# Optimization experiments

Hardware: AMD Instinct MI355X
Metric: run time of the kernel (lower is better)

Reference implementation:

```python
import jax, jax.numpy as jnp
import numpy as np

N_NODES = 50000
N_GRAPHS = 512


def _gcn_layer(x, src, dst, W, b):
    # DGL GraphConv, norm='both', allow_zero_in_degree=True
    n = x.shape[0]
    ones = jnp.ones(src.shape[0], x.dtype)
    deg_out = jnp.zeros(n, x.dtype).at[src].add(ones)
    deg_in = jnp.zeros(n, x.dtype).at[dst].add(ones)
    norm_out = jax.lax.rsqrt(jnp.maximum(deg_out, 1.0))
    norm_in = jax.lax.rsqrt(jnp.maximum(deg_in, 1.0))
    h = x * norm_out[:, None]
    agg = jax.ops.segment_sum(h[src], dst, num_segments=n)  # SpMM
    return (agg * norm_in[:, None]) @ W + b


def setup_inputs() -> dict:
    key = jax.random.key(0)
    ks = jax.random.split(key, 16)
    E = 800000
    inp = {
        'nid': jax.random.randint(ks[0], (N_NODES,), 0, 100000),
        'z': jax.random.randint(ks[1], (N_NODES,), 0, 1000),
        'src': jax.random.randint(ks[2], (E,), 0, N_NODES),
        'dst': jax.random.randint(ks[3], (E,), 0, N_NODES),
        'graph_id': jnp.sort(jax.random.randint(ks[4], (N_NODES,), 0, N_GRAPHS)),
        'init_embed': jax.random.normal(ks[5], (100000, 64), jnp.float32) * 0.1,
        'z_table': jax.random.normal(ks[6], (1000, 64), jnp.float32) * 0.1,
        'W0': jax.random.normal(ks[7], (128, 128), jnp.float32) * 0.1,
        'b0': jnp.zeros((128,), jnp.float32),
        'W1': jax.random.normal(ks[8], (128, 128), jnp.float32) * 0.1,
        'b1': jnp.zeros((128,), jnp.float32),
        'W2': jax.random.normal(ks[9], (128, 128), jnp.float32) * 0.1,
        'b2': jnp.zeros((128,), jnp.float32),
        'lin1_W': jax.random.normal(ks[10], (128, 128), jnp.float32) * 0.1,
        'lin1_b': jnp.zeros((128,), jnp.float32),
        'lin2_W': jax.random.normal(ks[11], (128, 200), jnp.float32) * 0.1,
        'lin2_b': jnp.zeros((200,), jnp.float32),
    }
    return inp


def reference(nid, z, src, dst, graph_id, init_embed, z_table, W0, b0, W1, b1, W2, b2, lin1_W, lin1_b, lin2_W, lin2_b):
    # node features: entity embedding lookup + structural label embedding, concat
    x = jnp.concatenate([init_embed[nid], z_table[z]], axis=1)  # [N, 128]
    # layers[:-1] with relu (dropout is identity in eval mode)
    x = jax.nn.relu(_gcn_layer(x, src, dst, W0, b0))
    x = jax.nn.relu(_gcn_layer(x, src, dst, W1, b1))
    x = _gcn_layer(x, src, dst, W2, b2)
    # SumPooling over subgraphs in the batch
    g = jax.ops.segment_sum(x, graph_id, num_segments=N_GRAPHS)  # [G, 128]
    h = jax.nn.relu(g @ lin1_W + lin1_b)
    return h @ lin2_W + lin2_b  # [G, num_rel]
```

## Files before the change

### kernel.cpp

```cpp
#include <hip/hip_runtime.h>
#include <hip/hip_bf16.h>


#define FEAT 128
#define NG 512
#define CH 128
#define NPMAX 12544
#define LDW 136

typedef __attribute__((ext_vector_type(8))) short bf16x8;
typedef __attribute__((ext_vector_type(4))) float f32x4;

__device__ __forceinline__ float bf2f(unsigned short u) {
    union { unsigned int i; float f; } v; v.i = ((unsigned int)u) << 16; return v.f;
}
__device__ __forceinline__ unsigned short f2bf(float f) {
    unsigned int u = __float_as_uint(f);
    return (unsigned short)((u + 0x7FFFu + ((u >> 16) & 1u)) >> 16);
}
__device__ __forceinline__ float lo16(unsigned u) { return __uint_as_float(u << 16); }
__device__ __forceinline__ float hi16(unsigned u) { return __uint_as_float(u & 0xFFFF0000u); }

__global__ __launch_bounds__(256) void k_hist(
        const int* __restrict__ src, const int* __restrict__ dst,
        unsigned* __restrict__ partial_out, unsigned* __restrict__ partial_in,
        int E, int NP, int Ec) {
    __shared__ unsigned h[NPMAX];
    int tid = threadIdx.x;
    int b = blockIdx.x;
    int c = b & (CH - 1);
    const int* __restrict__ arr = (b < CH) ? src : dst;
    unsigned* __restrict__ outp = ((b < CH) ? partial_out : partial_in) + (size_t)c * NP;
    for (int i = tid; i < NP; i += 256) h[i] = 0;
    __syncthreads();
    int e0 = c * Ec, e1 = min(E, e0 + Ec);
    for (int e = e0 + tid; e < e1; e += 256) {
        int v = arr[e];
        atomicAdd(&h[v >> 2], 1u << ((v & 3) * 8));
    }
    __syncthreads();
    for (int i = tid; i < NP; i += 256) outp[i] = h[i];
}

__global__ void k_merge(unsigned* __restrict__ partial_out, unsigned* __restrict__ partial_in,
                        int* __restrict__ cnt_in, float* __restrict__ norm_out,
                        float* __restrict__ norm_in, int N, int NP) {
    int w = blockIdx.x * blockDim.x + threadIdx.x;
    if (w >= NP) return;
    unsigned run_in = 0, run_out = 0;
    for (int c = 0; c < CH; c++) {
        size_t idx = (size_t)c * NP + w;
        unsigned v = partial_in[idx];
        partial_in[idx] = run_in;
        run_in += v;
        run_out += partial_out[idx];
    }
    #pragma unroll
    for (int j = 0; j < 4; j++) {
        int node = w * 4 + j;
        if (node < N) {
            unsigned di = (run_in  >> (j * 8)) & 255u;
            unsigned dd = (run_out >> (j * 8)) & 255u;
            cnt_in[node]   = (int)di;
            norm_in[node]  = rsqrtf(fmaxf((float)di, 1.0f));
            norm_out[node] = rsqrtf(fmaxf((float)dd, 1.0f));
        }
    }
}

__global__ void k_scan_local(const int* __restrict__ cnt, int* __restrict__ excl,
                             int* __restrict__ bsum, int N) {
    __shared__ int s[256];
    int x = threadIdx.x;
    int i = blockIdx.x * 256 + x;
    int v = (i < N) ? cnt[i] : 0;
    s[x] = v;
    __syncthreads();
    for (int off = 1; off < 256; off <<= 1) {
        int t = (x >= off) ? s[x - off] : 0;
        __syncthreads();
        s[x] += t;
        __syncthreads();
    }
    if (i < N) excl[i] = s[x] - v;
    if (x == 255) bsum[blockIdx.x] = s[255];
}

__global__ void k_scan_bsum_prep(int* __restrict__ bsum, int* __restrict__ boff, int nb,
                                 const float* __restrict__ W0, const float* __restrict__ W1,
                                 unsigned short* __restrict__ Wt0, unsigned short* __restrict__ Wt1) {
    if (blockIdx.x == 0) {
        __shared__ int s[256];
        int x = threadIdx.x;
        int v = (x < nb) ? bsum[x] : 0;
        s[x] = v;
        __syncthreads();
        for (int off = 1; off < 256; off <<= 1) {
            int t = (x >= off) ? s[x - off] : 0;
            __syncthreads();
            s[x] += t;
            __syncthreads();
        }
        if (x < nb) boff[x] = s[x] - v;
    } else {
        int t = ((int)blockIdx.x - 1) * 256 + threadIdx.x;
        if (t < 16384) {
            int n = t & 127, k = t >> 7;
            Wt0[n * 128 + k] = f2bf(W0[k * 128 + n]);
        } else {
            int t2 = t - 16384;
            int n = t2 & 127, k = t2 >> 7;
            Wt1[n * 128 + k] = f2bf(W1[k * 128 + n]);
        }
    }
}

__global__ void k_add_off(int* __restrict__ row_start, const int* __restrict__ boff, int N) {
    int i = blockIdx.x * blockDim.x + threadIdx.x;
    if (i < N) row_start[i] += boff[i >> 8];
}

__global__ __launch_bounds__(256) void k_fill_bx(
        const int* __restrict__ src, const int* __restrict__ dst,
        const int* __restrict__ row_start, const unsigned* __restrict__ partial_in,
        int* __restrict__ csr,
        const int* __restrict__ nid, const int* __restrict__ z,
        const float* __restrict__ emb, const float* __restrict__ zt,
        const float* __restrict__ nout, unsigned short* __restrict__ x,
        int N, int E, int NP, int Ec) {
    if ((int)blockIdx.x < CH) {
        __shared__ unsigned cur[NPMAX];
        int tid = threadIdx.x;
        int c = blockIdx.x;
        const unsigned* __restrict__ pre = partial_in + (size_t)c * NP;
        for (int i = tid; i < NP; i += 256) cur[i] = pre[i];
        __syncthreads();
        int e0 = c * Ec, e1 = min(E, e0 + Ec);
        for (int e = e0 + tid; e < e1; e += 256) {
            int d = dst[e], s = src[e];
            int sh = (d & 3) * 8;
            unsigned t = atomicAdd(&cur[d >> 2], 1u << sh);
            int off = (int)((t >> sh) & 255u);
            csr[row_start[d] + off] = s;
        }
    } else {
        int tid = ((int)blockIdx.x - CH) * 256 + threadIdx.x;
        int i = tid >> 5, q = tid & 31;
        if (i < N) {
            float4 v;
            if (q < 16) v = ((const float4*)emb)[(size_t)nid[i] * 16 + q];
            else        v = ((const float4*)zt)[(size_t)z[i] * 16 + (q - 16)];
            float w = nout[i];
            ushort4 u;
            u.x = f2bf(v.x * w); u.y = f2bf(v.y * w);
            u.z = f2bf(v.z * w); u.w = f2bf(v.w * w);
            ((ushort4*)x)[(size_t)i * 32 + q] = u;
        }
    }
}

#define GATHER_BODY                                                              \
    int tid = threadIdx.x;                                                       \
    int node = blockIdx.x * 16 + (tid >> 4);                                     \
    int ql = tid & 15;                                                           \
    if (node >= N) return;                                                       \
    int base = row_start[node];                                                  \
    int n = cnt_in[node];                                                        \
    float a0 = 0.f, a1 = 0.f, a2 = 0.f, a3 = 0.f;                                \
    float a4 = 0.f, a5 = 0.f, a6 = 0.f, a7 = 0.f;                                \
    const uint4* xp = (const uint4*)x;                       \
    for (int j0 = 0; j0 < n; j0 += 16) {                                         \
        int rem = n - j0;                                                        \
        int m = rem < 16 ? rem : 16;                                             \
        int e = csr[base + j0 + (ql < m ? ql : 0)];                              \
        int j = 0;                                                               \
        for (; j + 4 <= m; j += 4) {                                             \
            int s0 = __shfl(e, j + 0, 16), s1 = __shfl(e, j + 1, 16);            \
            int s2 = __shfl(e, j + 2, 16), s3 = __shfl(e, j + 3, 16);            \
            uint4 u0 = xp[(size_t)s0 * 16 + ql];                                 \
            uint4 u1 = xp[(size_t)s1 * 16 + ql];                                 \
            uint4 u2 = xp[(size_t)s2 * 16 + ql];                                 \
            uint4 u3 = xp[(size_t)s3 * 16 + ql];                                 \
            a0 += lo16(u0.x); a1 += hi16(u0.x); a2 += lo16(u0.y); a3 += hi16(u0.y); \
            a4 += lo16(u0.z); a5 += hi16(u0.z); a6 += lo16(u0.w); a7 += hi16(u0.w); \
            a0 += lo16(u1.x); a1 += hi16(u1.x); a2 += lo16(u1.y); a3 += hi16(u1.y); \
            a4 += lo16(u1.z); a5 += hi16(u1.z); a6 += lo16(u1.w); a7 += hi16(u1.w); \
            a0 += lo16(u2.x); a1 += hi16(u2.x); a2 += lo16(u2.y); a3 += hi16(u2.y); \
            a4 += lo16(u2.z); a5 += hi16(u2.z); a6 += lo16(u2.w); a7 += hi16(u2.w); \
            a0 += lo16(u3.x); a1 += hi16(u3.x); a2 += lo16(u3.y); a3 += hi16(u3.y); \
            a4 += lo16(u3.z); a5 += hi16(u3.z); a6 += lo16(u3.w); a7 += hi16(u3.w); \
        }                                                                        \
        for (; j < m; j++) {                                                     \
            int s = __shfl(e, j, 16);                                            \
            uint4 u = xp[(size_t)s * 16 + ql];                                   \
            a0 += lo16(u.x); a1 += hi16(u.x); a2 += lo16(u.y); a3 += hi16(u.y);  \
            a4 += lo16(u.z); a5 += hi16(u.z); a6 += lo16(u.w); a7 += hi16(u.w);  \
        }                                                                        \
    }                                                                            \
    float ni = nin[node];

__global__ __launch_bounds__(256) void k_gather_b(
        const unsigned short* __restrict__ x, const float* __restrict__ nin,
        const int* __restrict__ csr, const int* __restrict__ row_start,
        const int* __restrict__ cnt_in, unsigned short* __restrict__ aggB, int N) {
    GATHER_BODY
    uint4 o;
    o.x = (unsigned)f2bf(a0 * ni) | ((unsigned)f2bf(a1 * ni) << 16);
    o.y = (unsigned)f2bf(a2 * ni) | ((unsigned)f2bf(a3 * ni) << 16);
    o.z = (unsigned)f2bf(a4 * ni) | ((unsigned)f2bf(a5 * ni) << 16);
    o.w = (unsigned)f2bf(a6 * ni) | ((unsigned)f2bf(a7 * ni) << 16);
    ((uint4*)aggB)[(size_t)node * 16 + ql] = o;
}

__global__ __launch_bounds__(256) void k_gather(
        const unsigned short* __restrict__ x, const float* __restrict__ nin,
        const int* __restrict__ csr, const int* __restrict__ row_start,
        const int* __restrict__ cnt_in, float* __restrict__ agg, int N) {
    GATHER_BODY
    float4* ap = (float4*)(agg + (size_t)node * FEAT + ql * 8);
    ap[0] = make_float4(a0 * ni, a1 * ni, a2 * ni, a3 * ni);
    ap[1] = make_float4(a4 * ni, a5 * ni, a6 * ni, a7 * ni);
}

__global__ __launch_bounds__(256) void k_gemm_mfma(
        const unsigned short* __restrict__ aggB, const unsigned short* __restrict__ Wt,
        const float* __restrict__ bias, const float* __restrict__ nout,
        unsigned short* __restrict__ y, int N) {
    __shared__ unsigned short As[64 * LDW];
    __shared__ unsigned short Ws[128 * LDW];
    int tid = threadIdx.x;
    int nb = blockIdx.x * 64;

    for (int i = tid; i < 64 * 16; i += 256) {
        int row = i >> 4, seg = i & 15;
        int node = nb + row;
        ushort4 u0 = {0, 0, 0, 0}, u1 = u0;
        if (node < N) {
            const ushort4* p = (const ushort4*)(aggB + (size_t)node * 128 + seg * 8);
            u0 = p[0]; u1 = p[1];
        }
        ushort4* d = (ushort4*)(As + row * LDW + seg * 8);
        d[0] = u0; d[1] = u1;
    }
    for (int i = tid; i < 128 * 16; i += 256) {
        int row = i >> 4, seg = i & 15;
        const ushort4* p = (const ushort4*)(Wt + row * 128 + seg * 8);
        ushort4* d = (ushort4*)(Ws + row * LDW + seg * 8);
        d[0] = p[0]; d[1] = p[1];
    }
    __syncthreads();

    int lane = tid & 63;
    int m0 = (tid >> 6) * 16;
    int c = lane & 15, q = lane >> 4;

    const unsigned short* ap = As + (m0 + c) * LDW + q * 8;
    bf16x8 a0 = *(const bf16x8*)(ap);
    bf16x8 a1 = *(const bf16x8*)(ap + 32);
    bf16x8 a2 = *(const bf16x8*)(ap + 64);
    bf16x8 a3 = *(const bf16x8*)(ap + 96);

    #pragma unroll
    for (int nt = 0; nt < 8; nt++) {
        const unsigned short* wp = Ws + (nt * 16 + c) * LDW + q * 8;
        bf16x8 b0 = *(const bf16x8*)(wp);
        bf16x8 b1 = *(const bf16x8*)(wp + 32);
        bf16x8 b2 = *(const bf16x8*)(wp + 64);
        bf16x8 b3 = *(const bf16x8*)(wp + 96);
        float bb = bias[nt * 16 + c];
        f32x4 acc = {bb, bb, bb, bb};
        acc = __builtin_amdgcn_mfma_f32_16x16x32_bf16(a0, b0, acc, 0, 0, 0);
        acc = __builtin_amdgcn_mfma_f32_16x16x32_bf16(a1, b1, acc, 0, 0, 0);
        acc = __builtin_amdgcn_mfma_f32_16x16x32_bf16(a2, b2, acc, 0, 0, 0);
        acc = __builtin_amdgcn_mfma_f32_16x16x32_bf16(a3, b3, acc, 0, 0, 0);
        #pragma unroll
        for (int r = 0; r < 4; r++) {
            int row = m0 + q * 4 + r;
            float s = nout[min(nb + row, N - 1)];
            As[row * LDW + nt * 16 + c] = f2bf(fmaxf(acc[r], 0.f) * s);
        }
    }
    __syncthreads();

    for (int i = tid; i < 64 * 16; i += 256) {
        int row = i >> 4, seg = i & 15;
        int node = nb + row;
        if (node < N) {
            const ushort4* p = (const ushort4*)(As + row * LDW + seg * 8);
            ushort4* d = (ushort4*)(y + (size_t)node * 128 + seg * 8);
            d[0] = p[0]; d[1] = p[1];
        }
    }
}

__global__ __launch_bounds__(256) void k_head(
        const float* __restrict__ agg, const int* __restrict__ gid,
        const float* __restrict__ W2, const float* __restrict__ b2,
        const float* __restrict__ l1W, const float* __restrict__ l1b,
        const float* __restrict__ l2W, const float* __restrict__ l2b,
        float* __restrict__ out, int N) {
    __shared__ float g2[2][128];
    __shared__ float gs[128];
    __shared__ float ys[128];
    __shared__ float hs[128];
    int gi = blockIdx.x, tid = threadIdx.x;

    int lo = 0, hi = N;
    while (lo < hi) { int m = (lo + hi) >> 1; if (gid[m] < gi) lo = m + 1; else hi = m; }
    int s0 = lo;
    lo = 0; hi = N;
    while (lo < hi) { int m = (lo + hi) >> 1; if (gid[m] < gi + 1) lo = m + 1; else hi = m; }
    int e0 = lo;
    float cnt = (float)(e0 - s0);

    int t = tid >> 7, j = tid & 127;
    float p = 0.f;
    for (int i = s0 + t; i < e0; i += 2) p += agg[(size_t)i * FEAT + j];
    g2[t][j] = p;
    __syncthreads();
    if (tid < 128) gs[tid] = g2[0][tid] + g2[1][tid];
    __syncthreads();
    if (tid < 128) {
        float a = cnt * b2[tid];
        for (int k = 0; k < 128; k++) a += gs[k] * W2[(size_t)k * 128 + tid];
        ys[tid] = a;
    }
    __syncthreads();
    if (tid < 128) {
        float a = l1b[tid];
        for (int k = 0; k < 128; k++) a += ys[k] * l1W[(size_t)k * 128 + tid];
        hs[tid] = fmaxf(a, 0.f);
    }
    __syncthreads();
    if (tid < 200) {
        float a = l2b[tid];
        for (int k = 0; k < 128; k++) a += hs[k] * l2W[(size_t)k * 200 + tid];
        out[(size_t)gi * 200 + tid] = a;
    }
}

extern "C" void kernel_launch(void* const* d_in, const int* in_sizes, int n_in,
                              void* d_out, int out_size, void* d_ws, size_t ws_size,
                              hipStream_t stream) {
    const int*   nid = (const int*)d_in[0];
    const int*   z   = (const int*)d_in[1];
    const int*   src = (const int*)d_in[2];
    const int*   dst = (const int*)d_in[3];
    const int*   gid = (const int*)d_in[4];
    const float* emb = (const float*)d_in[5];
    const float* zt  = (const float*)d_in[6];
    const float* W0  = (const float*)d_in[7];
    const float* b0  = (const float*)d_in[8];
    const float* W1  = (const float*)d_in[9];
    const float* b1  = (const float*)d_in[10];
    const float* W2  = (const float*)d_in[11];
    const float* b2  = (const float*)d_in[12];
    const float* l1W = (const float*)d_in[13];
    const float* l1b = (const float*)d_in[14];
    const float* l2W = (const float*)d_in[15];
    const float* l2b = (const float*)d_in[16];
    float* out = (float*)d_out;

    const int N = in_sizes[0];
    const int E = in_sizes[2];
    const int NB = (N + 255) / 256;
    const int NP = (N + 3) / 4;
    const int Ec = (E + CH - 1) / CH;

    size_t NA = (size_t)((N + 63) & ~63);
    float* norm_out = (float*)d_ws;
    float* norm_in  = norm_out + NA;
    float* agg = norm_in + NA;
    unsigned short* xA   = (unsigned short*)(agg + (size_t)N * FEAT);
    unsigned short* xB   = xA + (size_t)N * FEAT;
    unsigned short* aggB = xB + (size_t)N * FEAT;
    unsigned short* Wt0  = aggB + (size_t)N * FEAT;
    unsigned short* Wt1  = Wt0 + 128 * 128;
    int* cnt_in    = (int*)(Wt1 + 128 * 128);
    int* row_start = cnt_in + NA;
    int* bsum      = row_start + NA;
    int* boff      = bsum + 256;
    unsigned* partial_out = (unsigned*)(boff + 256);
    unsigned* partial_in  = partial_out + (size_t)CH * NP;
    int* csr       = (int*)(partial_in + (size_t)CH * NP);

    k_hist<<<2 * CH, 256, 0, stream>>>(src, dst, partial_out, partial_in, E, NP, Ec);
    k_merge<<<(NP + 255) / 256, 256, 0, stream>>>(partial_out, partial_in, cnt_in,
                                                  norm_out, norm_in, N, NP);
    k_scan_local<<<NB, 256, 0, stream>>>(cnt_in, row_start, bsum, N);
    k_scan_bsum_prep<<<1 + 128, 256, 0, stream>>>(bsum, boff, NB, W0, W1, Wt0, Wt1);
    k_add_off<<<NB, 256, 0, stream>>>(row_start, boff, N);
    int XB = (N * 32 + 255) / 256;
    k_fill_bx<<<CH + XB, 256, 0, stream>>>(src, dst, row_start, partial_in, csr,
                                           nid, z, emb, zt, norm_out, xA, N, E, NP, Ec);

    int gat_blocks  = (N + 15) / 16;
    int gemm_blocks = (N + 63) / 64;

    k_gather_b<<<gat_blocks, 256, 0, stream>>>(xA, norm_in, csr, row_start, cnt_in, aggB, N);
    k_gemm_mfma<<<gemm_blocks, 256, 0, stream>>>(aggB, Wt0, b0, norm_out, xB, N);
    k_gather_b<<<gat_blocks, 256, 0, stream>>>(xB, norm_in, csr, row_start, cnt_in, aggB, N);
    k_gemm_mfma<<<gemm_blocks, 256, 0, stream>>>(aggB, Wt1, b1, norm_out, xA, N);
    k_gather<<<gat_blocks, 256, 0, stream>>>(xA, norm_in, csr, row_start, cnt_in, agg, N);

    k_head<<<NG, 256, 0, stream>>>(agg, gid, W2, b2, l1W, l1b, l2W, l2b, out, N);
}
```

Before: 310.7 us.

## Store CSR source indices as 16-bit and unroll gather by eight

The CSR neighbor index array is narrowed from int32 to uint16, halving index traffic in the fill and in the three gather passes. The gather inner loop gains an 8-way unrolled path so more row loads are in flight per iteration. Node ids run up to 50000, which fits in 16 bits, but this hard-codes the assumption that N stays below 65536. Wider unrolling also raises register pressure.

```diff
diff --git a/kernel.cpp b/kernel.cpp
--- a/kernel.cpp
+++ b/kernel.cpp
@@ -123,7 +123,7 @@
 __global__ __launch_bounds__(256) void k_fill_bx(
         const int* __restrict__ src, const int* __restrict__ dst,
         const int* __restrict__ row_start, const unsigned* __restrict__ partial_in,
-        int* __restrict__ csr,
+        unsigned short* __restrict__ csr,
         const int* __restrict__ nid, const int* __restrict__ z,
         const float* __restrict__ emb, const float* __restrict__ zt,
         const float* __restrict__ nout, unsigned short* __restrict__ x,
@@ -141,7 +141,7 @@
             int sh = (d & 3) * 8;
             unsigned t = atomicAdd(&cur[d >> 2], 1u << sh);
             int off = (int)((t >> sh) & 255u);
-            csr[row_start[d] + off] = s;
+            csr[row_start[d] + off] = (unsigned short)s;
         }
     } else {
         int tid = ((int)blockIdx.x - CH) * 256 + threadIdx.x;
@@ -158,6 +158,10 @@
         }
     }
 }
+
+#define ACC8(u)                                                                  \
+    a0 += lo16(u.x); a1 += hi16(u.x); a2 += lo16(u.y); a3 += hi16(u.y);          \
+    a4 += lo16(u.z); a5 += hi16(u.z); a6 += lo16(u.w); a7 += hi16(u.w);
 
 #define GATHER_BODY                                                              \
     int tid = threadIdx.x;                                                       \
@@ -172,8 +176,24 @@
     for (int j0 = 0; j0 < n; j0 += 16) {                                         \
         int rem = n - j0;                                                        \
         int m = rem < 16 ? rem : 16;                                             \
-        int e = csr[base + j0 + (ql < m ? ql : 0)];                              \
+        int e = (int)csr[base + j0 + (ql < m ? ql : 0)];                         \
         int j = 0;                                                               \
+        for (; j + 8 <= m; j += 8) {                                             \
+            int s0 = __shfl(e, j + 0, 16), s1 = __shfl(e, j + 1, 16);            \
+            int s2 = __shfl(e, j + 2, 16), s3 = __shfl(e, j + 3, 16);            \
+            int s4 = __shfl(e, j + 4, 16), s5 = __shfl(e, j + 5, 16);            \
+            int s6 = __shfl(e, j + 6, 16), s7 = __shfl(e, j + 7, 16);            \
+            uint4 u0 = xp[(size_t)s0 * 16 + ql];                                 \
+            uint4 u1 = xp[(size_t)s1 * 16 + ql];                                 \
+            uint4 u2 = xp[(size_t)s2 * 16 + ql];                                 \
+            uint4 u3 = xp[(size_t)s3 * 16 + ql];                                 \
+            uint4 u4 = xp[(size_t)s4 * 16 + ql];                                 \
+            uint4 u5 = xp[(size_t)s5 * 16 + ql];                                 \
+            uint4 u6 = xp[(size_t)s6 * 16 + ql];                                 \
+            uint4 u7 = xp[(size_t)s7 * 16 + ql];                                 \
+            ACC8(u0) ACC8(u1) ACC8(u2) ACC8(u3)                                  \
+            ACC8(u4) ACC8(u5) ACC8(u6) ACC8(u7)                                  \
+        }                                                                        \
         for (; j + 4 <= m; j += 4) {                                             \
             int s0 = __shfl(e, j + 0, 16), s1 = __shfl(e, j + 1, 16);            \
             int s2 = __shfl(e, j + 2, 16), s3 = __shfl(e, j + 3, 16);            \
@@ -181,27 +201,19 @@
             uint4 u1 = xp[(size_t)s1 * 16 + ql];                                 \
             uint4 u2 = xp[(size_t)s2 * 16 + ql];                                 \
             uint4 u3 = xp[(size_t)s3 * 16 + ql];                                 \
-            a0 += lo16(u0.x); a1 += hi16(u0.x); a2 += lo16(u0.y); a3 += hi16(u0.y); \
-            a4 += lo16(u0.z); a5 += hi16(u0.z); a6 += lo16(u0.w); a7 += hi16(u0.w); \
-            a0 += lo16(u1.x); a1 += hi16(u1.x); a2 += lo16(u1.y); a3 += hi16(u1.y); \
-            a4 += lo16(u1.z); a5 += hi16(u1.z); a6 += lo16(u1.w); a7 += hi16(u1.w); \
-            a0 += lo16(u2.x); a1 += hi16(u2.x); a2 += lo16(u2.y); a3 += hi16(u2.y); \
-            a4 += lo16(u2.z); a5 += hi16(u2.z); a6 += lo16(u2.w); a7 += hi16(u2.w); \
-            a0 += lo16(u3.x); a1 += hi16(u3.x); a2 += lo16(u3.y); a3 += hi16(u3.y); \
-            a4 += lo16(u3.z); a5 += hi16(u3.z); a6 += lo16(u3.w); a7 += hi16(u3.w); \
+            ACC8(u0) ACC8(u1) ACC8(u2) ACC8(u3)                                  \
         }                                                                        \
         for (; j < m; j++) {                                                     \
             int s = __shfl(e, j, 16);                                            \
             uint4 u = xp[(size_t)s * 16 + ql];                                   \
-            a0 += lo16(u.x); a1 += hi16(u.x); a2 += lo16(u.y); a3 += hi16(u.y);  \
-            a4 += lo16(u.z); a5 += hi16(u.z); a6 += lo16(u.w); a7 += hi16(u.w);  \
+            ACC8(u)                                                              \
         }                                                                        \
     }                                                                            \
     float ni = nin[node];
 
 __global__ __launch_bounds__(256) void k_gather_b(
         const unsigned short* __restrict__ x, const float* __restrict__ nin,
-        const int* __restrict__ csr, const int* __restrict__ row_start,
+        const unsigned short* __restrict__ csr, const int* __restrict__ row_start,
         const int* __restrict__ cnt_in, unsigned short* __restrict__ aggB, int N) {
     GATHER_BODY
     uint4 o;
@@ -214,7 +226,7 @@
 
 __global__ __launch_bounds__(256) void k_gather(
         const unsigned short* __restrict__ x, const float* __restrict__ nin,
-        const int* __restrict__ csr, const int* __restrict__ row_start,
+        const unsigned short* __restrict__ csr, const int* __restrict__ row_start,
         const int* __restrict__ cnt_in, float* __restrict__ agg, int N) {
     GATHER_BODY
     float4* ap = (float4*)(agg + (size_t)node * FEAT + ql * 8);
@@ -382,7 +394,7 @@
     int* boff      = bsum + 256;
     unsigned* partial_out = (unsigned*)(boff + 256);
     unsigned* partial_in  = partial_out + (size_t)CH * NP;
-    int* csr       = (int*)(partial_in + (size_t)CH * NP);
+    unsigned short* csr = (unsigned short*)(partial_in + (size_t)CH * NP);
 
     k_hist<<<2 * CH, 256, 0, stream>>>(src, dst, partial_out, partial_in, E, NP, Ec);
     k_merge<<<(NP + 255) / 256, 256, 0, stream>>>(partial_out, partial_in, cnt_in,
```

Measured after the change: 308.4 us. No clear change (-0.7%).
